# Kernel optimization log

Measured on AMD Instinct MI355X. Metric: run time of the kernel, lower is better.

Reference implementation:

```python
import jax, jax.numpy as jnp
import numpy as np

H = 512        # hidden_size
ENC = 2 * H    # encoder (context) feature dim
V = 10000      # vocab_size
B, T, L = 32, 500, 100
NEG_INF = -1e10


def setup_inputs() -> dict:
    key = jax.random.key(0)
    ks = jax.random.split(key, 16)
    sc = 0.02
    inp = {
        "h_batch": jax.random.normal(ks[0], (B, T, ENC), jnp.float32),
        "seq_lens": jax.random.randint(ks[1], (B,), 1, T + 1),
        "labels": jax.random.randint(ks[2], (B, L), 0, V),
        # content-based (additive) attention params
        "attn_Ws": jax.random.normal(ks[3], (H, H), jnp.float32) * sc,
        "attn_Wh": jax.random.normal(ks[4], (ENC, H), jnp.float32) * sc,
        "attn_b": jnp.zeros((H,), jnp.float32),
        "attn_v": jax.random.normal(ks[5], (H,), jnp.float32) * sc,
        # output path
        "W_sy": jax.random.normal(ks[6], (H, H), jnp.float32) * sc,
        "b_sy": jnp.zeros((H,), jnp.float32),
        "W_gy": jax.random.normal(ks[7], (ENC, H), jnp.float32) * sc,
        "b_gy": jnp.zeros((H,), jnp.float32),
        "W_yy": jax.random.normal(ks[8], (H, V), jnp.float32) * sc,
        "b_yy": jnp.zeros((V,), jnp.float32),
        # recurrence path
        "E_yr": jax.random.normal(ks[9], (V, 4 * H), jnp.float32) * sc,
        "W_sr": jax.random.normal(ks[10], (H, 4 * H), jnp.float32) * sc,
        "b_sr": jnp.zeros((4 * H,), jnp.float32),
        "W_gr": jax.random.normal(ks[11], (ENC, 4 * H), jnp.float32) * sc,
        "b_gr": jnp.zeros((4 * H,), jnp.float32),
    }
    return inp


def _func_lstm(rec_in, c):
    i, f, g, o = jnp.split(rec_in, 4, axis=-1)
    c_new = jax.nn.sigmoid(f) * c + jax.nn.sigmoid(i) * jnp.tanh(g)
    s_new = jax.nn.sigmoid(o) * jnp.tanh(c_new)
    return s_new, c_new


def reference(h_batch, seq_lens, labels, attn_Ws, attn_Wh, attn_b, attn_v,
              W_sy, b_sy, W_gy, b_gy, W_yy, b_yy,
              E_yr, W_sr, b_sr, W_gr, b_gr):
    Tlen = h_batch.shape[1]
    mask = jnp.arange(Tlen)[None, :] < seq_lens[:, None]          # [B,T]
    h_proj = jnp.einsum('bte,eh->bth', h_batch, attn_Wh) + attn_b  # precompute

    s0 = jnp.zeros((h_batch.shape[0], H), h_batch.dtype)
    c0 = jnp.zeros_like(s0)

    def step(carry, y_t):
        s, c = carry
        # content-based attention: e = v . tanh(Ws s + Wh h)
        e = jnp.einsum('bth,h->bt', jnp.tanh(h_proj + (s @ attn_Ws)[:, None, :]), attn_v)
        e = jnp.where(mask, e, NEG_INF)
        alpha = jax.nn.softmax(e, axis=-1)                         # [B,T]
        g = jnp.einsum('bt,bte->be', alpha, h_batch)               # [B,ENC]
        dec_feat = (g @ W_gy + b_gy) + (s @ W_sy + b_sy)
        y = jnp.tanh(dec_feat) @ W_yy + b_yy                       # [B,V]
        rec_in = E_yr[y_t] + (s @ W_sr + b_sr) + (g @ W_gr + b_gr) # [B,4H]
        s_new, c_new = _func_lstm(rec_in, c)
        return (s_new, c_new), y

    _, preds = jax.lax.scan(step, (s0, c0), labels.T)              # [L,B,V]
    return jnp.transpose(preds, (1, 0, 2))                         # [B,L,V]
```

## Files before the change

kernel.cpp:

```cpp
#include <hip/hip_runtime.h>
#include <cstdint>

#define B_   32
#define T_   500
#define H_   512
#define ENC_ 1024
#define V_   10000
#define L_   100
#define H4_  2048
#define NB_  256
#define NT_  512

#define OFF_HPROJ 0
#define OFF_WYYP  4096000
#define OFF_WRECP 6656000
#define OFF_WSB   10588160
#define OFF_S     10719232
#define OFF_DECTP 10735616
#define OFF_RACC  10752000
#define OFF_G0    10817536
#define OFF_G1    10850304
#define OFF_DEN   10883072
#define OFF_BAR   10883136
#define OFF_HB16  10883200
#define ZERO_CNT  163968

using bf16x8 = __attribute__((ext_vector_type(8))) short;
using f32x4  = __attribute__((ext_vector_type(4))) float;

__device__ __forceinline__ f32x4 mfma16(bf16x8 a, bf16x8 b, f32x4 c){
  return __builtin_amdgcn_mfma_f32_16x16x32_bf16(a, b, c, 0, 0, 0);
}
__device__ __forceinline__ unsigned short bfr(float f){
  unsigned x = __float_as_uint(f);
  return (unsigned short)((x + 0x7FFFu + ((x>>16)&1u)) >> 16);
}
__device__ __forceinline__ void bfsplit(float f, short& hi, short& lo){
  unsigned short h = bfr(f);
  float hf = __uint_as_float(((unsigned)h) << 16);
  hi = (short)h;
  lo = (short)bfr(f - hf);
}
__device__ __forceinline__ float bf2f(unsigned short u){
  return __uint_as_float(((unsigned)u) << 16);
}
__device__ __forceinline__ float ftanh(float x){
  float t = fminf(fmaxf(2.f*x, -30.f), 30.f);
  float e = __expf(t);
  return (e - 1.f) / (e + 1.f);
}
__device__ __forceinline__ float fsig(float x){
  float t = fminf(fmaxf(x, -30.f), 30.f);
  return 1.f / (1.f + __expf(-t));
}
__device__ __forceinline__ float gload(const float* p){
  return __hip_atomic_load((float*)p, __ATOMIC_RELAXED, __HIP_MEMORY_SCOPE_AGENT);
}
__device__ __forceinline__ void gstore(float* p, float v){
  __hip_atomic_store(p, v, __ATOMIC_RELAXED, __HIP_MEMORY_SCOPE_AGENT);
}
__device__ __forceinline__ void gstoreu(unsigned* p, unsigned v){
  __hip_atomic_store(p, v, __ATOMIC_RELAXED, __HIP_MEMORY_SCOPE_AGENT);
}
__device__ __forceinline__ void gload2(const float* p, float& a, float& b){
  unsigned long long u = __hip_atomic_load((const unsigned long long*)p,
                          __ATOMIC_RELAXED, __HIP_MEMORY_SCOPE_AGENT);
  a = __uint_as_float((unsigned)u);
  b = __uint_as_float((unsigned)(u >> 32));
}
__device__ __forceinline__ void gloadu2(const unsigned* p, unsigned& a, unsigned& b){
  unsigned long long u = __hip_atomic_load((const unsigned long long*)p,
                          __ATOMIC_RELAXED, __HIP_MEMORY_SCOPE_AGENT);
  a = (unsigned)u;
  b = (unsigned)(u >> 32);
}

__device__ __forceinline__ void gridbar(unsigned* bars, unsigned it){
  asm volatile("s_waitcnt vmcnt(0) lgkmcnt(0)" ::: "memory");
  __syncthreads();
  if (threadIdx.x == 0){
    unsigned* gc = bars + 1 + (blockIdx.x & 15);
    unsigned old = __hip_atomic_fetch_add(gc, 1u, __ATOMIC_RELAXED, __HIP_MEMORY_SCOPE_AGENT);
    if (old == it*16u + 15u)
      __hip_atomic_fetch_add(bars, 1u, __ATOMIC_RELAXED, __HIP_MEMORY_SCOPE_AGENT);
    while (__hip_atomic_load(bars, __ATOMIC_RELAXED, __HIP_MEMORY_SCOPE_AGENT) < (it+1u)*16u)
      __builtin_amdgcn_s_sleep(2);
  }
  __syncthreads();
  asm volatile("" ::: "memory");
}

__global__ void k_init(float* __restrict__ ws){
  int i = blockIdx.x * 256 + threadIdx.x;
  if (i < ZERO_CNT) ws[OFF_S + i] = 0.f;
}

__global__ void k_packWyy(const float* __restrict__ Wyy, float* __restrict__ ws){
  unsigned short* wp = (unsigned short*)(ws + OFF_WYYP);
  int t = blockIdx.x * 256 + threadIdx.x;
  if (t >= 625*16*64) return;
  int vt = t / 1024;
  int rem = t - vt*1024;
  int kc = rem >> 6, lane = rem & 63;
  int v  = vt*16 + (lane & 15);
  int k0 = kc*32 + ((lane >> 4) << 3);
  bf16x8 H;
  #pragma unroll
  for (int j = 0; j < 8; ++j) H[j] = (short)bfr(Wyy[(size_t)(k0+j)*V_ + v]);
  *(bf16x8*)(wp + ((size_t)(vt*16 + kc)*64 + lane)*8) = H;
}

__global__ void k_packWrec(const float* __restrict__ Wsy, const float* __restrict__ Wgy,
                           const float* __restrict__ Wsr, const float* __restrict__ Wgr,
                           float* __restrict__ ws){
  unsigned short* wp = (unsigned short*)(ws + OFF_WRECP);
  int t = blockIdx.x * 256 + threadIdx.x;
  if (t >= 160*48*64) return;
  int vt = t / (48*64);
  int rem = t - vt*(48*64);
  int kc = rem >> 6, lane = rem & 63;
  int col = vt*16 + (lane & 15);
  int k0  = kc*32 + ((lane >> 4) << 3);
  bf16x8 H;
  #pragma unroll
  for (int j = 0; j < 8; ++j){
    int k = k0 + j;
    float x;
    if (k < 512) x = (col < 512) ? Wsy[(size_t)k*512 + col] : Wsr[(size_t)k*2048 + (col-512)];
    else         x = (col < 512) ? Wgy[(size_t)(k-512)*512 + col] : Wgr[(size_t)(k-512)*2048 + (col-512)];
    H[j] = (short)bfr(x);
  }
  *(bf16x8*)(wp + ((size_t)(vt*48 + kc)*64 + lane)*8) = H;
}

__global__ void k_packWs(const float* __restrict__ Ws, float* __restrict__ ws){
  unsigned short* wp = (unsigned short*)(ws + OFF_WSB);
  int i = blockIdx.x * 256 + threadIdx.x;
  wp[i] = bfr(Ws[i]);
}

__global__ void k_packHB(const float* __restrict__ hb, float* __restrict__ ws){
  unsigned short* wp = (unsigned short*)(ws + OFF_HB16);
  int i = blockIdx.x * 256 + threadIdx.x;
  if (i < B_*T_*ENC_) wp[i] = bfr(hb[i]);
}

__global__ void k_hproj(const float* __restrict__ A, const float* __restrict__ W,
                        const float* __restrict__ bias, const int* __restrict__ lens,
                        float* __restrict__ ws){
  unsigned short* C = (unsigned short*)(ws + OFF_HPROJ);
  const int bm = blockIdx.x * 64;
  const int bn = blockIdx.y * 64;
  {
    int b0 = bm / T_, t0 = bm % T_;
    int b1 = (bm + 63) / T_;
    if (b0 == b1 && t0 >= lens[b0]) return;
  }
  __shared__ float As[64][33];
  __shared__ float Bs[32][68];
  const int tid = threadIdx.x;
  const int tx = tid & 15, ty = tid >> 4;
  float acc[4][4];
  #pragma unroll
  for (int i = 0; i < 4; ++i)
    #pragma unroll
    for (int j = 0; j < 4; ++j) acc[i][j] = 0.f;
  for (int k0 = 0; k0 < 1024; k0 += 32){
    for (int i = tid; i < 64*32; i += 256){
      int rr = i >> 5, cc = i & 31;
      As[rr][cc] = A[(size_t)(bm + rr) * 1024 + k0 + cc];
    }
    for (int i = tid; i < 32*64; i += 256){
      int rr = i >> 6, cc = i & 63;
      Bs[rr][cc] = W[(size_t)(k0 + rr) * 512 + bn + cc];
    }
    __syncthreads();
    #pragma unroll
    for (int kk = 0; kk < 32; ++kk){
      float a0 = As[ty*4+0][kk], a1 = As[ty*4+1][kk];
      float a2 = As[ty*4+2][kk], a3 = As[ty*4+3][kk];
      float4 b4 = *(const float4*)&Bs[kk][tx*4];
      acc[0][0] += a0*b4.x; acc[0][1] += a0*b4.y; acc[0][2] += a0*b4.z; acc[0][3] += a0*b4.w;
      acc[1][0] += a1*b4.x; acc[1][1] += a1*b4.y; acc[1][2] += a1*b4.z; acc[1][3] += a1*b4.w;
      acc[2][0] += a2*b4.x; acc[2][1] += a2*b4.y; acc[2][2] += a2*b4.z; acc[2][3] += a2*b4.w;
      acc[3][0] += a3*b4.x; acc[3][1] += a3*b4.y; acc[3][2] += a3*b4.z; acc[3][3] += a3*b4.w;
    }
    __syncthreads();
  }
  #pragma unroll
  for (int i = 0; i < 4; ++i){
    int m = bm + ty*4 + i;
    ushort4 o;
    o.x = bfr(acc[i][0] + bias[bn + tx*4 + 0]);
    o.y = bfr(acc[i][1] + bias[bn + tx*4 + 1]);
    o.z = bfr(acc[i][2] + bias[bn + tx*4 + 2]);
    o.w = bfr(acc[i][3] + bias[bn + tx*4 + 3]);
    *(ushort4*)&C[(size_t)m * 512 + bn + tx*4] = o;
  }
}

__global__ __launch_bounds__(NT_, 2) void k_persist(
    const int* __restrict__ lens,
    const int* __restrict__ labels, const float* __restrict__ av,
    const float* __restrict__ bsy, const float* __restrict__ bgy,
    const float* __restrict__ byy,
    const float* __restrict__ Eyr,
    const float* __restrict__ bsr, const float* __restrict__ bgr,
    float* __restrict__ out, float* __restrict__ ws)
{
  const int blk = blockIdx.x;
  const int tid = threadIdx.x;
  const int w   = tid >> 6;
  const int lane= tid & 63;
  unsigned* bars = (unsigned*)(ws + OFF_BAR);
  const unsigned short* wyyp  = (const unsigned short*)(ws + OFF_WYYP);
  const unsigned short* wrecp = (const unsigned short*)(ws + OFF_WRECP);
  const unsigned short* wsb   = (const unsigned short*)(ws + OFF_WSB);
  const unsigned short* hpB   = (const unsigned short*)(ws + OFF_HPROJ);
  const unsigned short* hb16  = (const unsigned short*)(ws + OFF_HB16);
  unsigned* dectP = (unsigned*)(ws + OFF_DECTP);
  unsigned* sP    = (unsigned*)(ws + OFF_S);
  __shared__ __align__(16) float smem[18688];

  const int arow  = lane & 15;
  const int klane = (lane >> 4) << 3;
  float c_reg = 0.f;

  for (int l = 0; l <= L_; ++l){
    const int p = l & 1;
    const int goff = p ? OFF_G1 : OFF_G0;
    if (blk < 157){
      if (l > 0){
        unsigned* dst = (unsigned*)smem;
        for (int i = tid; i < 8192; i += NT_){
          int row = i >> 8, k2 = (i & 255) << 1;
          unsigned a, b;
          gloadu2(dectP + row*H_ + k2, a, b);
          dst[row*516 + k2]     = a;
          dst[row*516 + k2 + 1] = b;
        }
        __syncthreads();
        const int kh = w & 1;
        const int vtslot = w >> 1;
        const int vt = blk*4 + vtslot;
        f32x4 a0 = {0.f,0.f,0.f,0.f}, a1 = {0.f,0.f,0.f,0.f};
        if (vt < 625){
          for (int kc2 = 0; kc2 < 8; ++kc2){
            const int kc = kh*8 + kc2;
            const int k0 = kc*32 + klane;
            bf16x8 Ahi0, Alo0, Ahi1, Alo1;
            {
              const unsigned* dp = dst + arow*516 + k0;
              uint4 qa = *(const uint4*)(dp);
              uint4 qb = *(const uint4*)(dp+4);
              unsigned q[8] = {qa.x,qa.y,qa.z,qa.w,qb.x,qb.y,qb.z,qb.w};
              #pragma unroll
              for (int j = 0; j < 8; ++j){
                Ahi0[j] = (short)(q[j] >> 16);
                Alo0[j] = (short)(q[j] & 0xFFFFu);
              }
            }
            {
              const unsigned* dp = dst + (arow+16)*516 + k0;
              uint4 qa = *(const uint4*)(dp);
              uint4 qb = *(const uint4*)(dp+4);
              unsigned q[8] = {qa.x,qa.y,qa.z,qa.w,qb.x,qb.y,qb.z,qb.w};
              #pragma unroll
              for (int j = 0; j < 8; ++j){
                Ahi1[j] = (short)(q[j] >> 16);
                Alo1[j] = (short)(q[j] & 0xFFFFu);
              }
            }
            bf16x8 Bv = *(const bf16x8*)(wyyp + ((size_t)(vt*16 + kc)*64 + lane)*8);
            a0 = mfma16(Ahi0, Bv, a0);
            a0 = mfma16(Alo0, Bv, a0);
            a1 = mfma16(Ahi1, Bv, a1);
            a1 = mfma16(Alo1, Bv, a1);
          }
        }
        float* red = smem + 16512;
        if (vt < 625 && kh == 0){
          #pragma unroll
          for (int r = 0; r < 4; ++r){
            red[vtslot*512 +       lane*4 + r] = a0[r];
            red[vtslot*512 + 256 + lane*4 + r] = a1[r];
          }
        }
        __syncthreads();
        if (vt < 625 && kh == 1){
          const int v = vt*16 + arow;
          const float bv = byy[v];
          const int lv = l - 1;
          #pragma unroll
          for (int r = 0; r < 4; ++r){
            const int row0 = ((lane >> 4) << 2) + r;
            float v0 = red[vtslot*512 +       lane*4 + r] + a0[r] + bv;
            float v1 = red[vtslot*512 + 256 + lane*4 + r] + a1[r] + bv;
            out[((size_t)(row0)*L_      + lv)*V_ + v] = v0;
            out[((size_t)(row0 + 16)*L_ + lv)*V_ + v] = v1;
          }
        }
        __syncthreads();
      }
    } else if (blk < 221){
      if (l < L_){
        const int u = blk - 157;
        const int b = u >> 1, half = u & 1;
        float* ssm  = smem;
        float* part = smem + 512;
        float* wsm  = smem + 2560;
        float* ex   = smem + 3072;
        float* pg   = smem + 3328;
        if (l == 0){
          ssm[tid] = 0.f;
          c_reg = 0.f;
        } else {
          const int h = tid;
          const float* ey = Eyr + (size_t)labels[b*L_ + (l-1)] * H4_;
          float ri = gload(&ws[OFF_RACC + b*H4_ + h])        + bsr[h]      + bgr[h]      + ey[h];
          float rf = gload(&ws[OFF_RACC + b*H4_ + 512 + h])  + bsr[512+h]  + bgr[512+h]  + ey[512+h];
          float rg = gload(&ws[OFF_RACC + b*H4_ + 1024 + h]) + bsr[1024+h] + bgr[1024+h] + ey[1024+h];
          float ro = gload(&ws[OFF_RACC + b*H4_ + 1536 + h]) + bsr[1536+h] + bgr[1536+h] + ey[1536+h];
          float cn = fsig(rf)*c_reg + fsig(ri)*ftanh(rg);
          float sn = fsig(ro)*ftanh(cn);
          c_reg = cn;
          if (half == 0){
            short h_, lo_; bfsplit(sn, h_, lo_);
            gstoreu(&sP[b*H_ + h], ((unsigned)(unsigned short)h_ << 16) | (unsigned)(unsigned short)lo_);
          }
          ssm[h] = sn;
        }
        __syncthreads();
        {
          const int colp = tid & 255;
          const int kh2  = tid >> 8;
          const int col0 = colp*2;
          const float* sp = ssm + kh2*256;
          const unsigned short* wb = wsb + (size_t)(kh2*256)*512 + col0;
          float acc0 = 0.f, acc1 = 0.f;
          for (int k = 0; k < 256; k += 8){
            float4 s0 = *(const float4*)&sp[k];
            float4 s1 = *(const float4*)&sp[k+4];
            unsigned wv[8];
            #pragma unroll
            for (int j = 0; j < 8; ++j)
              wv[j] = *(const unsigned*)&wb[(size_t)(k+j)*512];
            float sv[8] = {s0.x,s0.y,s0.z,s0.w,s1.x,s1.y,s1.z,s1.w};
            #pragma unroll
            for (int j = 0; j < 8; ++j){
              acc0 += sv[j] * bf2f((unsigned short)(wv[j] & 0xFFFFu));
              acc1 += sv[j] * bf2f((unsigned short)(wv[j] >> 16));
            }
          }
          part[kh2*1024 + col0]     = acc0;
          part[kh2*1024 + col0 + 1] = acc1;
        }
        __syncthreads();
        wsm[tid] = part[tid] + part[1024 + tid];
        __syncthreads();
        const int len = lens[b];
        {
          float avr[8], swr[8];
          #pragma unroll
          for (int j = 0; j < 8; ++j){
            avr[j] = av[lane*8 + j];
            swr[j] = wsm[lane*8 + j];
          }
          for (int t = 2*w + half; t < len; t += 16){
            bf16x8 hp = *(const bf16x8*)&hpB[(size_t)(b*T_ + t)*512 + lane*8];
            float sum = 0.f;
            #pragma unroll
            for (int j = 0; j < 8; ++j)
              sum += avr[j] * ftanh(bf2f((unsigned short)hp[j]) + swr[j]);
            #pragma unroll
            for (int off = 32; off > 0; off >>= 1) sum += __shfl_xor(sum, off, 64);
            if (lane == 0) ex[(t - half) >> 1] = __expf(sum);
          }
        }
        __syncthreads();
        const int n = (len - half + 1) >> 1;
        if (tid < 64){
          float s2 = 0.f;
          for (int i = tid; i < n; i += 64) s2 += ex[i];
          #pragma unroll
          for (int off = 32; off > 0; off >>= 1) s2 += __shfl_xor(s2, off, 64);
          if (tid == 0 && n > 0) atomicAdd(&ws[OFF_DEN + p*32 + b], s2);
        }
        {
          const int tg = tid >> 7;
          const int cl = tid & 127;
          const int col0 = cl*8;
          const unsigned short* hp = hb16 + (size_t)b*T_*ENC_ + col0;
          float acc[8] = {0.f,0.f,0.f,0.f,0.f,0.f,0.f,0.f};
          for (int idx = tg; idx < n; idx += 4){
            const int t = half + 2*idx;
            bf16x8 x = *(const bf16x8*)&hp[(size_t)t * ENC_];
            float a = ex[idx];
            #pragma unroll
            for (int j = 0; j < 8; ++j) acc[j] += a * bf2f((unsigned short)x[j]);
          }
          *(float4*)&pg[tg*1024 + col0]     = *(float4*)&acc[0];
          *(float4*)&pg[tg*1024 + col0 + 4] = *(float4*)&acc[4];
        }
        __syncthreads();
        if (tid < 256 && n > 0){
          const int c0 = tid*4;
          #pragma unroll
          for (int j = 0; j < 4; ++j){
            float s = pg[c0+j] + pg[1024+c0+j] + pg[2048+c0+j] + pg[3072+c0+j];
            atomicAdd(&ws[goff + b*ENC_ + c0 + j], s);
          }
        }
      }
    }
    if (l == L_) break;
    gridbar(bars, (unsigned)(l*2 + 0));

    if (blk < 160){
      const float invb0 = 1.f / gload(&ws[OFF_DEN + p*32 + arow]);
      const float invb1 = 1.f / gload(&ws[OFF_DEN + p*32 + arow + 16]);
      const int vt = blk;
      f32x4 acc0 = {0.f,0.f,0.f,0.f}, acc1 = {0.f,0.f,0.f,0.f};
      for (int j6 = 0; j6 < 6; ++j6){
        const int kc = w*6 + j6;
        const int k0 = kc*32 + klane;
        const bool isg = (k0 >= 512);
        bf16x8 Ahi0, Alo0, Ahi1, Alo1;
        if (!isg){
          unsigned q[8];
          const unsigned* dp = sP + arow*H_ + k0;
          gloadu2(dp+0, q[0], q[1]);
          gloadu2(dp+2, q[2], q[3]);
          gloadu2(dp+4, q[4], q[5]);
          gloadu2(dp+6, q[6], q[7]);
          #pragma unroll
          for (int j = 0; j < 8; ++j){
            Ahi0[j] = (short)(q[j] >> 16);
            Alo0[j] = (short)(q[j] & 0xFFFFu);
          }
          const unsigned* dp1 = sP + (arow+16)*H_ + k0;
          gloadu2(dp1+0, q[0], q[1]);
          gloadu2(dp1+2, q[2], q[3]);
          gloadu2(dp1+4, q[4], q[5]);
          gloadu2(dp1+6, q[6], q[7]);
          #pragma unroll
          for (int j = 0; j < 8; ++j){
            Ahi1[j] = (short)(q[j] >> 16);
            Alo1[j] = (short)(q[j] & 0xFFFFu);
          }
        } else {
          {
            const float* src = &ws[goff + arow*ENC_ + (k0 - 512)];
            float x[8];
            gload2(src+0, x[0], x[1]);
            gload2(src+2, x[2], x[3]);
            gload2(src+4, x[4], x[5]);
            gload2(src+6, x[6], x[7]);
            #pragma unroll
            for (int j = 0; j < 8; ++j){
              short h, lo; bfsplit(x[j]*invb0, h, lo);
              Ahi0[j] = h; Alo0[j] = lo;
            }
          }
          {
            const float* src = &ws[goff + (arow+16)*ENC_ + (k0 - 512)];
            float x[8];
            gload2(src+0, x[0], x[1]);
            gload2(src+2, x[2], x[3]);
            gload2(src+4, x[4], x[5]);
            gload2(src+6, x[6], x[7]);
            #pragma unroll
            for (int j = 0; j < 8; ++j){
              short h, lo; bfsplit(x[j]*invb1, h, lo);
              Ahi1[j] = h; Alo1[j] = lo;
            }
          }
        }
        bf16x8 Bv = *(const bf16x8*)(wrecp + ((size_t)(vt*48 + kc)*64 + lane)*8);
        acc0 = mfma16(Ahi0, Bv, acc0);
        acc0 = mfma16(Alo0, Bv, acc0);
        acc1 = mfma16(Ahi1, Bv, acc1);
        acc1 = mfma16(Alo1, Bv, acc1);
      }
      #pragma unroll
      for (int r = 0; r < 4; ++r){
        smem[(w*2 + 0)*256 + lane*4 + r] = acc0[r];
        smem[(w*2 + 1)*256 + lane*4 + r] = acc1[r];
      }
      __syncthreads();
      {
        const int bt = tid >> 8, r8 = tid & 255;
        float v = 0.f;
        #pragma unroll
        for (int w8 = 0; w8 < 8; ++w8)
          v += smem[(w8*2 + bt)*256 + r8];
        const int ln = r8 >> 2, rr = r8 & 3;
        const int row = bt*16 + ((ln >> 4) << 2) + rr;
        const int col = blk*16 + (ln & 15);
        if (col < 512){
          float t = ftanh(v + bsy[col] + bgy[col]);
          unsigned short hi_ = bfr(t);
          unsigned short lo_ = bfr(t - bf2f(hi_));
          gstoreu(&dectP[row*H_ + col], ((unsigned)hi_ << 16) | lo_);
        } else {
          gstore(&ws[OFF_RACC + row*H4_ + (col - 512)], v);
        }
      }
    } else if (blk < 176){
      const int zoff = p ? OFF_G0 : OFF_G1;
      for (int i = (blk - 160)*NT_ + tid; i < B_*ENC_; i += 16*NT_)
        gstore(&ws[zoff + i], 0.f);
      if (blk == 160 && tid < 32)
        gstore(&ws[OFF_DEN + (p^1)*32 + tid], 0.f);
    }
    gridbar(bars, (unsigned)(l*2 + 1));
  }
}

extern "C" void kernel_launch(void* const* d_in, const int* in_sizes, int n_in,
                              void* d_out, int out_size, void* d_ws, size_t ws_size,
                              hipStream_t stream){
  const float* h_batch = (const float*)d_in[0];
  const int*   seq_lens= (const int*)d_in[1];
  const int*   labels  = (const int*)d_in[2];
  const float* attn_Ws = (const float*)d_in[3];
  const float* attn_Wh = (const float*)d_in[4];
  const float* attn_b  = (const float*)d_in[5];
  const float* attn_v  = (const float*)d_in[6];
  const float* W_sy    = (const float*)d_in[7];
  const float* b_sy    = (const float*)d_in[8];
  const float* W_gy    = (const float*)d_in[9];
  const float* b_gy    = (const float*)d_in[10];
  const float* W_yy    = (const float*)d_in[11];
  const float* b_yy    = (const float*)d_in[12];
  const float* E_yr    = (const float*)d_in[13];
  const float* W_sr    = (const float*)d_in[14];
  const float* b_sr    = (const float*)d_in[15];
  const float* W_gr    = (const float*)d_in[16];
  const float* b_gr    = (const float*)d_in[17];
  float* out = (float*)d_out;
  float* ws  = (float*)d_ws;

  k_init    <<<641, 256, 0, stream>>>(ws);
  k_packWyy <<<2500, 256, 0, stream>>>(W_yy, ws);
  k_packWrec<<<1920, 256, 0, stream>>>(W_sy, W_gy, W_sr, W_gr, ws);
  k_packWs  <<<1024, 256, 0, stream>>>(attn_Ws, ws);
  k_packHB  <<<64000, 256, 0, stream>>>(h_batch, ws);
  k_hproj   <<<dim3(250, 8), 256, 0, stream>>>(h_batch, attn_Wh, attn_b, seq_lens, ws);

  void* kargs[] = {
    (void*)&seq_lens, (void*)&labels, (void*)&attn_v,
    (void*)&b_sy, (void*)&b_gy, (void*)&b_yy,
    (void*)&E_yr, (void*)&b_sr, (void*)&b_gr,
    (void*)&out, (void*)&ws
  };
  hipLaunchCooperativeKernel((void*)k_persist, dim3(NB_), dim3(NT_), kargs, 0, stream);
}
```

Before: 9.318 ms.

## Double persistent-kernel block size to 1024 threads and split K across more waves

Raises the persistent kernel's block size from 512 to 1024 threads (one block per CU) and redistributes work so each wave handles a smaller K slice. This covers the vocab projection, the recurrence GEMM, the attention scoring and context loops, and the Ws matvec. Partial sums are reduced through shared memory over more slices. The aim is to shorten the per-step serial critical path of the persistent recurrence by using more waves per block. In exchange there are more reduction passes and synchronisations, and register pressure per thread may be higher.

```diff
diff --git a/kernel.cpp b/kernel.cpp
--- a/kernel.cpp
+++ b/kernel.cpp
@@ -9,7 +9,7 @@
 #define L_   100
 #define H4_  2048
 #define NB_  256
-#define NT_  512
+#define NT_  1024
 
 #define OFF_HPROJ 0
 #define OFF_WYYP  4096000
@@ -199,7 +199,7 @@
   }
 }
 
-__global__ __launch_bounds__(NT_, 2) void k_persist(
+__global__ __launch_bounds__(NT_, 1) void k_persist(
     const int* __restrict__ lens,
     const int* __restrict__ labels, const float* __restrict__ av,
     const float* __restrict__ bsy, const float* __restrict__ bgy,
@@ -220,7 +220,7 @@
   const unsigned short* hb16  = (const unsigned short*)(ws + OFF_HB16);
   unsigned* dectP = (unsigned*)(ws + OFF_DECTP);
   unsigned* sP    = (unsigned*)(ws + OFF_S);
-  __shared__ __align__(16) float smem[18688];
+  __shared__ __align__(16) float smem[16512];
 
   const int arow  = lane & 15;
   const int klane = (lane >> 4) << 3;
@@ -240,13 +240,14 @@
           dst[row*516 + k2 + 1] = b;
         }
         __syncthreads();
-        const int kh = w & 1;
-        const int vtslot = w >> 1;
+        const int vtslot = w >> 2;
+        const int khq    = w & 3;
         const int vt = blk*4 + vtslot;
         f32x4 a0 = {0.f,0.f,0.f,0.f}, a1 = {0.f,0.f,0.f,0.f};
         if (vt < 625){
-          for (int kc2 = 0; kc2 < 8; ++kc2){
-            const int kc = kh*8 + kc2;
+          #pragma unroll
+          for (int kc2 = 0; kc2 < 4; ++kc2){
+            const int kc = khq*4 + kc2;
             const int k0 = kc*32 + klane;
             bf16x8 Ahi0, Alo0, Ahi1, Alo1;
             {
@@ -278,26 +279,31 @@
             a1 = mfma16(Alo1, Bv, a1);
           }
         }
-        float* red = smem + 16512;
-        if (vt < 625 && kh == 0){
-          #pragma unroll
-          for (int r = 0; r < 4; ++r){
-            red[vtslot*512 +       lane*4 + r] = a0[r];
-            red[vtslot*512 + 256 + lane*4 + r] = a1[r];
-          }
-        }
-        __syncthreads();
-        if (vt < 625 && kh == 1){
-          const int v = vt*16 + arow;
-          const float bv = byy[v];
-          const int lv = l - 1;
-          #pragma unroll
-          for (int r = 0; r < 4; ++r){
-            const int row0 = ((lane >> 4) << 2) + r;
-            float v0 = red[vtslot*512 +       lane*4 + r] + a0[r] + bv;
-            float v1 = red[vtslot*512 + 256 + lane*4 + r] + a1[r] + bv;
-            out[((size_t)(row0)*L_      + lv)*V_ + v] = v0;
-            out[((size_t)(row0 + 16)*L_ + lv)*V_ + v] = v1;
+        __syncthreads();
+        #pragma unroll
+        for (int r = 0; r < 4; ++r){
+          smem[((vtslot*4 + khq)*2 + 0)*256 + lane*4 + r] = a0[r];
+          smem[((vtslot*4 + khq)*2 + 1)*256 + lane*4 + r] = a1[r];
+        }
+        __syncthreads();
+        const int lv = l - 1;
+        #pragma unroll
+        for (int oo = 0; oo < 2; ++oo){
+          const int q   = tid + oo*NT_;
+          const int vts = q >> 9;
+          const int rem = q & 511;
+          const int bt  = rem >> 8;
+          const int r8  = rem & 255;
+          const int vto = blk*4 + vts;
+          if (vto < 625){
+            float v = 0.f;
+            #pragma unroll
+            for (int kq = 0; kq < 4; ++kq)
+              v += smem[((vts*4 + kq)*2 + bt)*256 + r8];
+            const int ln = r8 >> 2, rr = r8 & 3;
+            const int row = bt*16 + ((ln >> 4) << 2) + rr;
+            const int vcol = vto*16 + (ln & 15);
+            out[((size_t)row*L_ + lv)*V_ + vcol] = v + byy[vcol];
           }
         }
         __syncthreads();
@@ -308,55 +314,50 @@
         const int b = u >> 1, half = u & 1;
         float* ssm  = smem;
         float* part = smem + 512;
-        float* wsm  = smem + 2560;
-        float* ex   = smem + 3072;
-        float* pg   = smem + 3328;
+        float* wsm  = smem + 1536;
+        float* ex   = smem + 2048;
+        float* pg   = smem + 2304;
         if (l == 0){
-          ssm[tid] = 0.f;
-          c_reg = 0.f;
+          if (tid < 512){ ssm[tid] = 0.f; c_reg = 0.f; }
         } else {
-          const int h = tid;
-          const float* ey = Eyr + (size_t)labels[b*L_ + (l-1)] * H4_;
-          float ri = gload(&ws[OFF_RACC + b*H4_ + h])        + bsr[h]      + bgr[h]      + ey[h];
-          float rf = gload(&ws[OFF_RACC + b*H4_ + 512 + h])  + bsr[512+h]  + bgr[512+h]  + ey[512+h];
-          float rg = gload(&ws[OFF_RACC + b*H4_ + 1024 + h]) + bsr[1024+h] + bgr[1024+h] + ey[1024+h];
-          float ro = gload(&ws[OFF_RACC + b*H4_ + 1536 + h]) + bsr[1536+h] + bgr[1536+h] + ey[1536+h];
-          float cn = fsig(rf)*c_reg + fsig(ri)*ftanh(rg);
-          float sn = fsig(ro)*ftanh(cn);
-          c_reg = cn;
-          if (half == 0){
-            short h_, lo_; bfsplit(sn, h_, lo_);
-            gstoreu(&sP[b*H_ + h], ((unsigned)(unsigned short)h_ << 16) | (unsigned)(unsigned short)lo_);
-          }
-          ssm[h] = sn;
+          if (tid < 512){
+            const int h = tid;
+            const float* ey = Eyr + (size_t)labels[b*L_ + (l-1)] * H4_;
+            float ri = gload(&ws[OFF_RACC + b*H4_ + h])        + bsr[h]      + bgr[h]      + ey[h];
+            float rf = gload(&ws[OFF_RACC + b*H4_ + 512 + h])  + bsr[512+h]  + bgr[512+h]  + ey[512+h];
+            float rg = gload(&ws[OFF_RACC + b*H4_ + 1024 + h]) + bsr[1024+h] + bgr[1024+h] + ey[1024+h];
+            float ro = gload(&ws[OFF_RACC + b*H4_ + 1536 + h]) + bsr[1536+h] + bgr[1536+h] + ey[1536+h];
+            float cn = fsig(rf)*c_reg + fsig(ri)*ftanh(rg);
+            float sn = fsig(ro)*ftanh(cn);
+            c_reg = cn;
+            if (half == 0){
+              short h_, lo_; bfsplit(sn, h_, lo_);
+              gstoreu(&sP[b*H_ + h], ((unsigned)(unsigned short)h_ << 16) | (unsigned)(unsigned short)lo_);
+            }
+            ssm[h] = sn;
+          }
         }
         __syncthreads();
         {
-          const int colp = tid & 255;
-          const int kh2  = tid >> 8;
-          const int col0 = colp*2;
-          const float* sp = ssm + kh2*256;
-          const unsigned short* wb = wsb + (size_t)(kh2*256)*512 + col0;
-          float acc0 = 0.f, acc1 = 0.f;
+          const int col  = tid & 511;
+          const int ksec = tid >> 9;
+          const float* sp = ssm + ksec*256;
+          const unsigned short* wb = wsb + (size_t)(ksec*256)*512 + col;
+          float acc = 0.f;
           for (int k = 0; k < 256; k += 8){
             float4 s0 = *(const float4*)&sp[k];
             float4 s1 = *(const float4*)&sp[k+4];
-            unsigned wv[8];
+            float wv[8];
             #pragma unroll
             for (int j = 0; j < 8; ++j)
-              wv[j] = *(const unsigned*)&wb[(size_t)(k+j)*512];
-            float sv[8] = {s0.x,s0.y,s0.z,s0.w,s1.x,s1.y,s1.z,s1.w};
-            #pragma unroll
-            for (int j = 0; j < 8; ++j){
-              acc0 += sv[j] * bf2f((unsigned short)(wv[j] & 0xFFFFu));
-              acc1 += sv[j] * bf2f((unsigned short)(wv[j] >> 16));
-            }
-          }
-          part[kh2*1024 + col0]     = acc0;
-          part[kh2*1024 + col0 + 1] = acc1;
-        }
-        __syncthreads();
-        wsm[tid] = part[tid] + part[1024 + tid];
+              wv[j] = bf2f(wb[(size_t)(k+j)*512]);
+            acc += s0.x*wv[0] + s0.y*wv[1] + s0.z*wv[2] + s0.w*wv[3]
+                 + s1.x*wv[4] + s1.y*wv[5] + s1.z*wv[6] + s1.w*wv[7];
+          }
+          part[ksec*512 + col] = acc;
+        }
+        __syncthreads();
+        if (tid < 512) wsm[tid] = part[tid] + part[512 + tid];
         __syncthreads();
         const int len = lens[b];
         {
@@ -366,7 +367,7 @@
             avr[j] = av[lane*8 + j];
             swr[j] = wsm[lane*8 + j];
           }
-          for (int t = 2*w + half; t < len; t += 16){
+          for (int t = 2*w + half; t < len; t += 32){
             bf16x8 hp = *(const bf16x8*)&hpB[(size_t)(b*T_ + t)*512 + lane*8];
             float sum = 0.f;
             #pragma unroll
@@ -392,7 +393,7 @@
           const int col0 = cl*8;
           const unsigned short* hp = hb16 + (size_t)b*T_*ENC_ + col0;
           float acc[8] = {0.f,0.f,0.f,0.f,0.f,0.f,0.f,0.f};
-          for (int idx = tg; idx < n; idx += 4){
+          for (int idx = tg; idx < n; idx += 8){
             const int t = half + 2*idx;
             bf16x8 x = *(const bf16x8*)&hp[(size_t)t * ENC_];
             float a = ex[idx];
@@ -407,7 +408,8 @@
           const int c0 = tid*4;
           #pragma unroll
           for (int j = 0; j < 4; ++j){
-            float s = pg[c0+j] + pg[1024+c0+j] + pg[2048+c0+j] + pg[3072+c0+j];
+            float s = pg[c0+j] + pg[1024+c0+j] + pg[2048+c0+j] + pg[3072+c0+j]
+                    + pg[4096+c0+j] + pg[5120+c0+j] + pg[6144+c0+j] + pg[7168+c0+j];
             atomicAdd(&ws[goff + b*ENC_ + c0 + j], s);
           }
         }
@@ -421,8 +423,9 @@
       const float invb1 = 1.f / gload(&ws[OFF_DEN + p*32 + arow + 16]);
       const int vt = blk;
       f32x4 acc0 = {0.f,0.f,0.f,0.f}, acc1 = {0.f,0.f,0.f,0.f};
-      for (int j6 = 0; j6 < 6; ++j6){
-        const int kc = w*6 + j6;
+      #pragma unroll
+      for (int j3 = 0; j3 < 3; ++j3){
+        const int kc = w*3 + j3;
         const int k0 = kc*32 + klane;
         const bool isg = (k0 >= 512);
         bf16x8 Ahi0, Alo0, Ahi1, Alo1;
@@ -488,12 +491,12 @@
         smem[(w*2 + 1)*256 + lane*4 + r] = acc1[r];
       }
       __syncthreads();
-      {
+      if (tid < 512){
         const int bt = tid >> 8, r8 = tid & 255;
         float v = 0.f;
         #pragma unroll
-        for (int w8 = 0; w8 < 8; ++w8)
-          v += smem[(w8*2 + bt)*256 + r8];
+        for (int w16 = 0; w16 < 16; ++w16)
+          v += smem[(w16*2 + bt)*256 + r8];
         const int ln = r8 >> 2, rr = r8 & 3;
         const int row = bt*16 + ((ln >> 4) << 2) + rr;
         const int col = blk*16 + (ln & 15);
```

Result: slower. 18.07 ms (+93.9%).
